# Optimization experiments

Hardware: AMD Instinct MI355X
Metric: run time of the kernel (lower is better)

## Reference

```python
import jax, jax.numpy as jnp
import numpy as np

B, S, H, D = 4, 4096, 1024, 64

def setup_inputs() -> dict:
    key = jax.random.key(0)
    ks = jax.random.split(key, 10)
    return {
        "query": jax.random.normal(ks[0], (B, S, H), jnp.float32),
        "key": jax.random.normal(ks[1], (B, S, H), jnp.float32),
        "value": jax.random.normal(ks[2], (B, S, H), jnp.float32),
        "mask": jax.random.randint(ks[3], (B, S), 0, 2, jnp.int32),
        "Wq": jax.random.normal(ks[4], (H, D), jnp.float32) * 0.02,
        "bq": jax.random.normal(ks[5], (D,), jnp.float32) * 0.02,
        "Wk": jax.random.normal(ks[6], (H, D), jnp.float32) * 0.02,
        "bk": jax.random.normal(ks[7], (D,), jnp.float32) * 0.02,
        "Wv": jax.random.normal(ks[8], (H, D), jnp.float32) * 0.02,
        "bv": jax.random.normal(ks[9], (D,), jnp.float32) * 0.02,
    }

def reference(query, key, value, mask, Wq, bq, Wk, bk, Wv, bv):
    # single-head projections: [B,S,H] @ [H,D] -> [B,S,D]
    q = query @ Wq + bq
    k = key @ Wk + bk
    v = value @ Wv + bv
    scale = 1.0 / np.sqrt(D).astype(np.float32)
    # [B,Sq,Sk] score matrix (faithful to the unfused original)
    scores = jnp.einsum('bqd,bkd->bqk', q, k) * scale
    # mask [B,Sk] broadcast over query dim; masked positions -> -1e9
    scores = jnp.where(mask[:, None, :] == 0, jnp.float32(-1e9), scores)
    att = jax.nn.softmax(scores, axis=-1)
    # dropout prob = 0.0 -> identity
    return jnp.einsum('bqk,bkd->bqd', att, v)
```

## Files before the change

kernel.cpp:

```cpp
#include <hip/hip_runtime.h>
#include <hip/hip_bf16.h>
#include <stdint.h>


typedef __bf16 bf16;
typedef __bf16 bf16x8 __attribute__((ext_vector_type(8)));
typedef float f32x16 __attribute__((ext_vector_type(16)));

union B8 { uint4 u; bf16x8 v; uint32_t w[4]; };

#define AS1 __attribute__((address_space(1)))
#define AS3 __attribute__((address_space(3)))

__device__ __forceinline__ void async16(const void* g, void* l) {
  __builtin_amdgcn_global_load_lds((AS1 void*)(g), (AS3 void*)(l), 16, 0, 0);
}

#define KSC 0.18033688011112042f

__global__ void setup_kernel(const float* __restrict__ Wq, const float* __restrict__ Wk,
                             const float* __restrict__ Wv, const int* __restrict__ mask,
                             bf16* __restrict__ wT, float* __restrict__ biasArr)
{
  int item = blockIdx.x * 256 + threadIdx.x;
  if (item < 24576) {
    int mat = item >> 13;
    int rem = item & 8191;
    int n   = rem >> 7;
    int c   = rem & 127;
    const float* W = (mat == 0) ? Wq : (mat == 1) ? Wk : Wv;
    union { bf16 b[8]; uint4 u; } pk;
    #pragma unroll
    for (int j = 0; j < 8; ++j)
      pk.b[j] = (bf16)W[(c * 8 + j) * 64 + n];
    bf16* o = wT + mat * 65536;
    *(uint4*)(o + n * 1024 + c * 8) = pk.u;
  } else {
    int i = (item - 24576) << 2;
    const int4 m = *(const int4*)(mask + i);
    float4 b;
    b.x = m.x ? 0.0f : -1e30f;
    b.y = m.y ? 0.0f : -1e30f;
    b.z = m.z ? 0.0f : -1e30f;
    b.w = m.w ? 0.0f : -1e30f;
    *(float4*)(biasArr + i) = b;
  }
}

__global__ __launch_bounds__(128) void proj_kernel(
    const float* __restrict__ Xq, const float* __restrict__ Xk, const float* __restrict__ Xv,
    const bf16* __restrict__ wT,
    const float* __restrict__ bq, const float* __restrict__ bk, const float* __restrict__ bv,
    bf16* __restrict__ qo, bf16* __restrict__ ko, bf16* __restrict__ vTo)
{
  const int bx = blockIdx.x;
  const int mat = bx >> 9;
  const int m0 = (bx & 511) << 5;
  const float* X    = (mat == 0) ? Xq : (mat == 1) ? Xk : Xv;
  const float* bias = (mat == 0) ? bq : (mat == 1) ? bk : bv;
  const bf16* w = wT + mat * 65536;

  __shared__ __align__(16) float xbuf[2][32 * 64];
  __shared__ __align__(16) bf16 cs[32 * 64];

  const int tid  = threadIdx.x;
  const int wv   = tid >> 6;
  const int lane = tid & 63;
  const int half = lane >> 5;
  const int ln   = lane & 31;

  const int drow = lane >> 4;
  const int dcl  = lane & 15;

  const float* xb = X + (size_t)m0 * 1024;
  const bf16*  w0 = w + ((wv << 5) + ln) * 1024 + half * 8;

  float b0v = bias[(wv << 5) + ln];

  float4 sx0, sx1, sx2, sx3;
  uint4  sw0, sw1, sw2, sw3;
  uint4  cw0, cw1, cw2, cw3;

  #define LX1(dst, i_, j)                                                  \
    { int ii_ = (wv << 2) + (i_);                                          \
      int row_ = ii_ * 4 + drow;                                           \
      int sc_ = (dcl & 8) | ((dcl ^ (row_ & 7)) & 7);                      \
      dst = *(const float4*)(xb + (size_t)(j) * 64 + (size_t)row_ * 1024 + sc_ * 4); }
  #define LOADX(j)  LX1(sx0, 0, j) LX1(sx1, 1, j) LX1(sx2, 2, j) LX1(sx3, 3, j)

  #define LW1(dst, s_, j)  { dst = *(const uint4*)(w0 + (j) * 64 + (s_) * 16); }
  #define LOADW_S(j) LW1(sw0, 0, j) LW1(sw1, 1, j) LW1(sw2, 2, j) LW1(sw3, 3, j)
  #define LOADW_C(j) LW1(cw0, 0, j) LW1(cw1, 1, j) LW1(cw2, 2, j) LW1(cw3, 3, j)

  #define WX1(src, i_, dptr)                                               \
    { int ii_ = (wv << 2) + (i_);                                          \
      *(float4*)((dptr) + ii_ * 256 + lane * 4) = src; }
  #define WRITEX(dptr) WX1(sx0, 0, dptr) WX1(sx1, 1, dptr) WX1(sx2, 2, dptr) WX1(sx3, 3, dptr)

  #define CST(s_, WREG)                                                    \
    { int lc_ = (s_) * 4 + half * 2;                                       \
      int p0_ = (lc_ & 8) | ((lc_ ^ (ln & 7)) & 7);                        \
      int p1_ = ((lc_ + 1) & 8) | (((lc_ + 1) ^ (ln & 7)) & 7);            \
      float4 fa_ = *(const float4*)(xl + ln * 64 + p0_ * 4);               \
      float4 fb_ = *(const float4*)(xl + ln * 64 + p1_ * 4);               \
      union { bf16 b[8]; bf16x8 v; } af_;                                  \
      af_.b[0] = (bf16)fa_.x; af_.b[1] = (bf16)fa_.y;                      \
      af_.b[2] = (bf16)fa_.z; af_.b[3] = (bf16)fa_.w;                      \
      af_.b[4] = (bf16)fb_.x; af_.b[5] = (bf16)fb_.y;                      \
      af_.b[6] = (bf16)fb_.z; af_.b[7] = (bf16)fb_.w;                      \
      B8 wa_; wa_.u = WREG;                                                \
      acc = __builtin_amdgcn_mfma_f32_32x32x16_bf16(af_.v, wa_.v, acc, 0, 0, 0); }

  LOADX(0);
  LOADW_C(0);
  { float* dp = &xbuf[0][0]; WRITEX(dp); }
  asm volatile("s_waitcnt lgkmcnt(0)" ::: "memory");
  __builtin_amdgcn_s_barrier();

  f32x16 acc = {};

  for (int c = 0; c < 16; ++c) {
    if (c < 15) {
      LOADX(c + 1);
      LOADW_S(c + 1);
    }
    const float* xl = &xbuf[c & 1][0];
    CST(0, cw0) CST(1, cw1) CST(2, cw2) CST(3, cw3)
    if (c < 15) {
      { float* dp = &xbuf[(c + 1) & 1][0]; WRITEX(dp); }
      asm volatile("s_waitcnt lgkmcnt(0)" ::: "memory");
      __builtin_amdgcn_s_barrier();
      cw0 = sw0; cw1 = sw1; cw2 = sw2; cw3 = sw3;
    }
  }

  #undef LX1
  #undef LOADX
  #undef LW1
  #undef LOADW_S
  #undef LOADW_C
  #undef WX1
  #undef WRITEX
  #undef CST

  #pragma unroll
  for (int r = 0; r < 16; ++r) {
    int mrow = (r & 3) + 8 * (r >> 2) + 4 * half;
    cs[mrow * 64 + (wv << 5) + ln] = (bf16)(acc[r] + b0v);
  }
  __syncthreads();

  if (mat < 2) {
    bf16* gout = (mat == 0) ? qo : ko;
    #pragma unroll
    for (int p = 0; p < 2; ++p) {
      int id = p * 128 + tid;
      int r = id >> 3;
      int c = id & 7;
      int phys = c ^ (r & 7);
      *(uint4*)(gout + (size_t)(m0 + r) * 64 + phys * 8) = *(const uint4*)(cs + r * 64 + c * 8);
    }
  } else {
    int batch = m0 >> 12;
    int sk = m0 & 4095;
    int tb = sk & ~63;
    int halfTile = (sk >> 5) & 1;
    #pragma unroll
    for (int p = 0; p < 2; ++p) {
      int id = p * 128 + tid;
      int d = id >> 2;
      int j = id & 3;
      union { bf16 b[8]; uint4 u; } pk;
      #pragma unroll
      for (int t = 0; t < 8; ++t) pk.b[t] = cs[(j * 8 + t) * 64 + d];
      int cl = halfTile * 4 + j;
      int phys = cl ^ (d & 7);
      *(uint4*)(vTo + ((size_t)batch * 64 + d) * 4096 + tb + phys * 8) = pk.u;
    }
  }
}

__global__ __launch_bounds__(256, 2) void flash_kernel(
    const bf16* __restrict__ qb, const bf16* __restrict__ kb, const bf16* __restrict__ vT,
    const float* __restrict__ biasArr, float* __restrict__ out)
{
  __shared__ __align__(16) char smem[65536];
  bf16* ksb = (bf16*)smem;
  bf16* vsb = (bf16*)(smem + 32768);

  const int tid = threadIdx.x;
  const int lane = tid & 63;
  const int wv = tid >> 6;
  const int half = lane >> 5;
  const int ln = lane & 31;

  const int batch = blockIdx.x >> 6;
  const int q0 = (blockIdx.x & 63) << 6;

  bf16x8 qf[2][4];
  const bf16* qbase = qb + ((size_t)batch * 4096 + q0) * 64;
  #pragma unroll
  for (int qk = 0; qk < 2; ++qk)
  #pragma unroll
  for (int s = 0; s < 4; ++s) {
    int qq = (qk << 5) + ln;
    int phys = (2 * s + half) ^ (qq & 7);
    B8 t; t.u = *(const uint4*)(qbase + qq * 64 + phys * 8);
    qf[qk][s] = t.v;
  }

  f32x16 acc[2][2] = {{{}, {}}, {{}, {}}};
  float den0 = 0.f, den1 = 0.f;

  bf16* kds = ksb + wv * 4096;
  bf16* vds = vsb + wv * 4096;
  const bf16* kgb = kb + (size_t)batch * 4096 * 64;
  const bf16* vgb = vT + (size_t)batch * 64 * 4096;
  const float* barr = biasArr + batch * 4096;

  for (int it = 0; it < 16; ++it) {
    const int key0 = wv * 1024 + it * 64;
    __syncthreads();
    const bf16* ksrc = kgb + (size_t)key0 * 64;
    #pragma unroll
    for (int i = 0; i < 8; ++i)
      async16((const char*)ksrc + i * 1024 + lane * 16, (char*)kds + i * 1024);
    const bf16* vsrc = vgb + key0;
    #pragma unroll
    for (int i = 0; i < 8; ++i)
      async16((const char*)vsrc + ((size_t)(i * 8 + (lane >> 3)) * 4096 + (lane & 7) * 8) * 2,
              (char*)vds + i * 1024);
    __syncthreads();

    #pragma unroll
    for (int st = 0; st < 2; ++st) {
      f32x16 s0 = {};
      f32x16 s1 = {};
      #pragma unroll
      for (int s = 0; s < 4; ++s) {
        int key = (st << 5) + ln;
        B8 af; af.u = *(const uint4*)(kds + key * 64 + (((2 * s + half) ^ (key & 7)) << 3));
        s0 = __builtin_amdgcn_mfma_f32_32x32x16_bf16(af.v, qf[0][s], s0, 0, 0, 0);
        s1 = __builtin_amdgcn_mfma_f32_32x32x16_bf16(af.v, qf[1][s], s1, 0, 0, 0);
      }
      float bb[16];
      #pragma unroll
      for (int g = 0; g < 4; ++g)
        *(float4*)&bb[4 * g] = *(const float4*)(barr + key0 + (st << 5) + 8 * g + (half << 2));
      uint32_t pk0[8], pk1[8];
      #pragma unroll
      for (int i = 0; i < 8; ++i) {
        float a0 = __builtin_amdgcn_exp2f(fmaf(s0[2 * i],     KSC, bb[2 * i]));
        float a1 = __builtin_amdgcn_exp2f(fmaf(s0[2 * i + 1], KSC, bb[2 * i + 1]));
        float c0 = __builtin_amdgcn_exp2f(fmaf(s1[2 * i],     KSC, bb[2 * i]));
        float c1 = __builtin_amdgcn_exp2f(fmaf(s1[2 * i + 1], KSC, bb[2 * i + 1]));
        den0 += a0 + a1;
        den1 += c0 + c1;
        union { bf16 b[2]; uint32_t u; } u0, u1;
        u0.b[0] = (bf16)a0; u0.b[1] = (bf16)a1;
        u1.b[0] = (bf16)c0; u1.b[1] = (bf16)c1;
        pk0[i] = u0.u; pk1[i] = u1.u;
      }
      uint32_t xp0[8], xp1[8];
      #pragma unroll
      for (int i = 0; i < 8; ++i) {
        xp0[i] = (uint32_t)__shfl_xor((int)pk0[i], 32);
        xp1[i] = (uint32_t)__shfl_xor((int)pk1[i], 32);
      }
      #pragma unroll
      for (int t = 0; t < 2; ++t) {
        B8 p0f, p1f;
        p0f.w[0] = half ? xp0[4 * t + 2] : pk0[4 * t];
        p0f.w[1] = half ? xp0[4 * t + 3] : pk0[4 * t + 1];
        p0f.w[2] = half ? pk0[4 * t + 2] : xp0[4 * t];
        p0f.w[3] = half ? pk0[4 * t + 3] : xp0[4 * t + 1];
        p1f.w[0] = half ? xp1[4 * t + 2] : pk1[4 * t];
        p1f.w[1] = half ? xp1[4 * t + 3] : pk1[4 * t + 1];
        p1f.w[2] = half ? pk1[4 * t + 2] : xp1[4 * t];
        p1f.w[3] = half ? pk1[4 * t + 3] : xp1[4 * t + 1];
        #pragma unroll
        for (int dh = 0; dh < 2; ++dh) {
          int d = (dh << 5) + ln;
          B8 vf; vf.u = *(const uint4*)(vds + d * 64 +
                          ((((st << 2) + (t << 1) + half) ^ (d & 7)) << 3));
          acc[0][dh] = __builtin_amdgcn_mfma_f32_32x32x16_bf16(vf.v, p0f.v, acc[0][dh], 0, 0, 0);
          acc[1][dh] = __builtin_amdgcn_mfma_f32_32x32x16_bf16(vf.v, p1f.v, acc[1][dh], 0, 0, 0);
        }
      }
    }
  }

  den0 += __shfl_xor(den0, 32);
  den1 += __shfl_xor(den1, 32);

  float* nb = (float*)smem;
  float* dn = (float*)(smem + 34816);

  __syncthreads();
  if (wv >= 2) {
    float* mynb = nb + (wv - 2) * 4352;
    #pragma unroll
    for (int qk = 0; qk < 2; ++qk)
    #pragma unroll
    for (int dh = 0; dh < 2; ++dh)
    #pragma unroll
    for (int g = 0; g < 4; ++g) {
      int q = (qk << 5) + ln;
      int d = 8 * g + (half << 2) + (dh << 5);
      f32x16 a = acc[qk][dh];
      *(float4*)(mynb + q * 68 + d) = make_float4(a[4*g], a[4*g+1], a[4*g+2], a[4*g+3]);
    }
    if (half == 0) {
      dn[(wv - 2) * 64 + ln]      = den0;
      dn[(wv - 2) * 64 + 32 + ln] = den1;
    }
  }
  __syncthreads();
  if (wv < 2) {
    float* pb = nb + wv * 4352;
    #pragma unroll
    for (int qk = 0; qk < 2; ++qk)
    #pragma unroll
    for (int dh = 0; dh < 2; ++dh)
    #pragma unroll
    for (int g = 0; g < 4; ++g) {
      int q = (qk << 5) + ln;
      int d = 8 * g + (half << 2) + (dh << 5);
      float4 t = *(const float4*)(pb + q * 68 + d);
      acc[qk][dh][4*g+0] += t.x; acc[qk][dh][4*g+1] += t.y;
      acc[qk][dh][4*g+2] += t.z; acc[qk][dh][4*g+3] += t.w;
    }
    den0 += dn[wv * 64 + ln];
    den1 += dn[wv * 64 + 32 + ln];
  }
  __syncthreads();
  if (wv < 2) {
    float* mynb = nb + wv * 4352;
    #pragma unroll
    for (int qk = 0; qk < 2; ++qk)
    #pragma unroll
    for (int dh = 0; dh < 2; ++dh)
    #pragma unroll
    for (int g = 0; g < 4; ++g) {
      int q = (qk << 5) + ln;
      int d = 8 * g + (half << 2) + (dh << 5);
      f32x16 a = acc[qk][dh];
      *(float4*)(mynb + q * 68 + d) = make_float4(a[4*g], a[4*g+1], a[4*g+2], a[4*g+3]);
    }
    if (half == 0) {
      dn[wv * 64 + ln]      = den0;
      dn[wv * 64 + 32 + ln] = den1;
    }
  }
  __syncthreads();
  #pragma unroll
  for (int p = 0; p < 4; ++p) {
    int i = p * 256 + tid;
    int qq = i >> 4;
    int d4 = (i & 15) << 2;
    float4 A = *(const float4*)(nb + qq * 68 + d4);
    float4 Bv = *(const float4*)(nb + 4352 + qq * 68 + d4);
    float dd = dn[qq] + dn[64 + qq];
    float inv = 1.0f / dd;
    float4 o = make_float4((A.x + Bv.x) * inv, (A.y + Bv.y) * inv,
                           (A.z + Bv.z) * inv, (A.w + Bv.w) * inv);
    *(float4*)(out + ((size_t)batch * 4096 + q0 + qq) * 64 + d4) = o;
  }
}

extern "C" void kernel_launch(void* const* d_in, const int* in_sizes, int n_in,
                              void* d_out, int out_size, void* d_ws, size_t ws_size,
                              hipStream_t stream)
{
  const float* query = (const float*)d_in[0];
  const float* key   = (const float*)d_in[1];
  const float* value = (const float*)d_in[2];
  const int*   mask  = (const int*)d_in[3];
  const float* Wq    = (const float*)d_in[4];
  const float* bq    = (const float*)d_in[5];
  const float* Wk    = (const float*)d_in[6];
  const float* bk    = (const float*)d_in[7];
  const float* Wv    = (const float*)d_in[8];
  const float* bv    = (const float*)d_in[9];
  float* out = (float*)d_out;

  bf16* qb = (bf16*)d_ws;
  bf16* kb = qb + 1048576;
  bf16* vT = kb + 1048576;
  bf16* wT = vT + 1048576;
  float* biasArr = (float*)((char*)d_ws + 3 * 2097152 + 393216);

  setup_kernel<<<112, 256, 0, stream>>>(Wq, Wk, Wv, mask, wT, biasArr);
  proj_kernel<<<1536, 128, 0, stream>>>(query, key, value, wT, bq, bk, bv, qb, kb, vT);
  flash_kernel<<<256, 256, 0, stream>>>(qb, kb, vT, biasArr, out);
}
```

Measured before the change: 271.5 us.

## Stage full 32x1024 X tile in LDS as bf16 before projection MFMA loop

The projection kernel no longer streams X in 64-column fp32 chunks through a double buffer with a barrier per chunk. Each wave now loads its 16 rows of X with long contiguous per-lane reads, converts them to bf16 once, and writes them into a 64KB swizzled LDS buffer. After a single barrier, the MFMA loop reads ready-made bf16 fragments. This removes 15 barriers and repeated per-chunk conversion, at the cost of 64KB of LDS per block, which limits occupancy, and no overlap between the X load and compute.

```diff
diff --git a/kernel.cpp b/kernel.cpp
--- a/kernel.cpp
+++ b/kernel.cpp
@@ -60,8 +60,8 @@
   const float* bias = (mat == 0) ? bq : (mat == 1) ? bk : bv;
   const bf16* w = wT + mat * 65536;
 
-  __shared__ __align__(16) float xbuf[2][32 * 64];
-  __shared__ __align__(16) bf16 cs[32 * 64];
+  __shared__ __align__(16) char psm[65536];
+  bf16* cs = (bf16*)psm;
 
   const int tid  = threadIdx.x;
   const int wv   = tid >> 6;
@@ -69,79 +69,76 @@
   const int half = lane >> 5;
   const int ln   = lane & 31;
 
-  const int drow = lane >> 4;
-  const int dcl  = lane & 15;
-
-  const float* xb = X + (size_t)m0 * 1024;
-  const bf16*  w0 = w + ((wv << 5) + ln) * 1024 + half * 8;
-
+  const bf16* w0 = w + ((wv << 5) + ln) * 1024 + half * 8;
   float b0v = bias[(wv << 5) + ln];
 
-  float4 sx0, sx1, sx2, sx3;
-  uint4  sw0, sw1, sw2, sw3;
-  uint4  cw0, cw1, cw2, cw3;
-
-  #define LX1(dst, i_, j)                                                  \
-    { int ii_ = (wv << 2) + (i_);                                          \
-      int row_ = ii_ * 4 + drow;                                           \
-      int sc_ = (dcl & 8) | ((dcl ^ (row_ & 7)) & 7);                      \
-      dst = *(const float4*)(xb + (size_t)(j) * 64 + (size_t)row_ * 1024 + sc_ * 4); }
-  #define LOADX(j)  LX1(sx0, 0, j) LX1(sx1, 1, j) LX1(sx2, 2, j) LX1(sx3, 3, j)
-
+  const float* xrow = X + (size_t)(m0 + (wv << 4)) * 1024 + lane * 16;
+  const int c16a = lane * 2;
+  const int c16b = lane * 2 + 1;
+  const int gx   = (lane >> 2) & 7;
+
+  float4 a0, a1, a2, a3, b0, b1, b2, b3;
+
+  #define LDROW(s0, s1, s2, s3, rr)                                        \
+    { const float* p_ = xrow + (size_t)(rr) * 1024;                        \
+      s0 = *(const float4*)(p_);      s1 = *(const float4*)(p_ + 4);       \
+      s2 = *(const float4*)(p_ + 8);  s3 = *(const float4*)(p_ + 12); }
+
+  #define WRROW(s0, s1, s2, s3, rr)                                        \
+    { int r_ = (wv << 4) + (rr);                                           \
+      int pa_ = (c16a & ~7) | ((c16a ^ (r_ & 7) ^ gx) & 7);                \
+      int pb_ = (c16b & ~7) | ((c16b ^ (r_ & 7) ^ gx) & 7);                \
+      union { bf16 b[8]; uint4 q; } ua_, ub_;                              \
+      ua_.b[0] = (bf16)s0.x; ua_.b[1] = (bf16)s0.y;                        \
+      ua_.b[2] = (bf16)s0.z; ua_.b[3] = (bf16)s0.w;                        \
+      ua_.b[4] = (bf16)s1.x; ua_.b[5] = (bf16)s1.y;                        \
+      ua_.b[6] = (bf16)s1.z; ua_.b[7] = (bf16)s1.w;                        \
+      ub_.b[0] = (bf16)s2.x; ub_.b[1] = (bf16)s2.y;                        \
+      ub_.b[2] = (bf16)s2.z; ub_.b[3] = (bf16)s2.w;                        \
+      ub_.b[4] = (bf16)s3.x; ub_.b[5] = (bf16)s3.y;                        \
+      ub_.b[6] = (bf16)s3.z; ub_.b[7] = (bf16)s3.w;                        \
+      *(uint4*)(psm + r_ * 2048 + pa_ * 16) = ua_.q;                       \
+      *(uint4*)(psm + r_ * 2048 + pb_ * 16) = ub_.q; }
+
+  LDROW(a0, a1, a2, a3, 0)
+  for (int rr = 0; rr < 16; rr += 2) {
+    LDROW(b0, b1, b2, b3, rr + 1)
+    WRROW(a0, a1, a2, a3, rr)
+    if (rr < 14) LDROW(a0, a1, a2, a3, rr + 2)
+    WRROW(b0, b1, b2, b3, rr + 1)
+  }
+  #undef LDROW
+  #undef WRROW
+
+  __syncthreads();
+
+  uint4 cw0, cw1, cw2, cw3, sw0, sw1, sw2, sw3;
   #define LW1(dst, s_, j)  { dst = *(const uint4*)(w0 + (j) * 64 + (s_) * 16); }
+  #define LOADW_C(j) LW1(cw0, 0, j) LW1(cw1, 1, j) LW1(cw2, 2, j) LW1(cw3, 3, j)
   #define LOADW_S(j) LW1(sw0, 0, j) LW1(sw1, 1, j) LW1(sw2, 2, j) LW1(sw3, 3, j)
-  #define LOADW_C(j) LW1(cw0, 0, j) LW1(cw1, 1, j) LW1(cw2, 2, j) LW1(cw3, 3, j)
-
-  #define WX1(src, i_, dptr)                                               \
-    { int ii_ = (wv << 2) + (i_);                                          \
-      *(float4*)((dptr) + ii_ * 256 + lane * 4) = src; }
-  #define WRITEX(dptr) WX1(sx0, 0, dptr) WX1(sx1, 1, dptr) WX1(sx2, 2, dptr) WX1(sx3, 3, dptr)
-
-  #define CST(s_, WREG)                                                    \
-    { int lc_ = (s_) * 4 + half * 2;                                       \
-      int p0_ = (lc_ & 8) | ((lc_ ^ (ln & 7)) & 7);                        \
-      int p1_ = ((lc_ + 1) & 8) | (((lc_ + 1) ^ (ln & 7)) & 7);            \
-      float4 fa_ = *(const float4*)(xl + ln * 64 + p0_ * 4);               \
-      float4 fb_ = *(const float4*)(xl + ln * 64 + p1_ * 4);               \
-      union { bf16 b[8]; bf16x8 v; } af_;                                  \
-      af_.b[0] = (bf16)fa_.x; af_.b[1] = (bf16)fa_.y;                      \
-      af_.b[2] = (bf16)fa_.z; af_.b[3] = (bf16)fa_.w;                      \
-      af_.b[4] = (bf16)fb_.x; af_.b[5] = (bf16)fb_.y;                      \
-      af_.b[6] = (bf16)fb_.z; af_.b[7] = (bf16)fb_.w;                      \
+
+  #define CSTN(c_, s_, WREG)                                               \
+    { int c16_ = (c_) * 8 + (s_) * 2 + half;                               \
+      int phys_ = (c16_ & ~7) | ((c16_ ^ (ln & 7) ^ ((c_) & 7)) & 7);      \
+      B8 af_; af_.u = *(const uint4*)(psm + ln * 2048 + phys_ * 16);       \
       B8 wa_; wa_.u = WREG;                                                \
       acc = __builtin_amdgcn_mfma_f32_32x32x16_bf16(af_.v, wa_.v, acc, 0, 0, 0); }
 
-  LOADX(0);
+  f32x16 acc = {};
+
   LOADW_C(0);
-  { float* dp = &xbuf[0][0]; WRITEX(dp); }
-  asm volatile("s_waitcnt lgkmcnt(0)" ::: "memory");
-  __builtin_amdgcn_s_barrier();
-
-  f32x16 acc = {};
-
   for (int c = 0; c < 16; ++c) {
-    if (c < 15) {
-      LOADX(c + 1);
-      LOADW_S(c + 1);
-    }
-    const float* xl = &xbuf[c & 1][0];
-    CST(0, cw0) CST(1, cw1) CST(2, cw2) CST(3, cw3)
-    if (c < 15) {
-      { float* dp = &xbuf[(c + 1) & 1][0]; WRITEX(dp); }
-      asm volatile("s_waitcnt lgkmcnt(0)" ::: "memory");
-      __builtin_amdgcn_s_barrier();
-      cw0 = sw0; cw1 = sw1; cw2 = sw2; cw3 = sw3;
-    }
-  }
-
-  #undef LX1
-  #undef LOADX
+    if (c < 15) { LOADW_S(c + 1) }
+    CSTN(c, 0, cw0) CSTN(c, 1, cw1) CSTN(c, 2, cw2) CSTN(c, 3, cw3)
+    if (c < 15) { cw0 = sw0; cw1 = sw1; cw2 = sw2; cw3 = sw3; }
+  }
+
   #undef LW1
+  #undef LOADW_C
   #undef LOADW_S
-  #undef LOADW_C
-  #undef WX1
-  #undef WRITEX
-  #undef CST
+  #undef CSTN
+
+  __syncthreads();
 
   #pragma unroll
   for (int r = 0; r < 16; ++r) {
```

Result: no change. 276.3 us (+1.8%).

## Enlarge projection tile to 64 rows and stage weights in shared memory

Applied to the files above, without the earlier changes.

The projection kernel now computes 64x64 output tiles with 256 threads, so each block reads half as many weight passes per activation row. Both the X and W chunks are staged through double-buffered swizzled LDS, and X is converted to bf16 before the LDS write rather than after the read. The weight matrix was previously loaded straight from global into registers by each wave. This cuts redundant weight traffic and LDS bytes, but uses more LDS per block and launches fewer blocks.

```diff
diff --git a/kernel.cpp b/kernel.cpp
--- a/kernel.cpp
+++ b/kernel.cpp
@@ -47,106 +47,113 @@
   }
 }
 
-__global__ __launch_bounds__(128) void proj_kernel(
+__global__ __launch_bounds__(256) void proj_kernel(
     const float* __restrict__ Xq, const float* __restrict__ Xk, const float* __restrict__ Xv,
     const bf16* __restrict__ wT,
     const float* __restrict__ bq, const float* __restrict__ bk, const float* __restrict__ bv,
     bf16* __restrict__ qo, bf16* __restrict__ ko, bf16* __restrict__ vTo)
 {
   const int bx = blockIdx.x;
-  const int mat = bx >> 9;
-  const int m0 = (bx & 511) << 5;
+  const int mat = bx >> 8;
+  const int m0 = (bx & 255) << 6;
   const float* X    = (mat == 0) ? Xq : (mat == 1) ? Xk : Xv;
   const float* bias = (mat == 0) ? bq : (mat == 1) ? bk : bv;
-  const bf16* w = wT + mat * 65536;
-
-  __shared__ __align__(16) float xbuf[2][32 * 64];
-  __shared__ __align__(16) bf16 cs[32 * 64];
+  const bf16* wm = wT + mat * 65536;
+
+  __shared__ __align__(16) char xsm[2][8192];
+  __shared__ __align__(16) char wsm[2][8192];
+  __shared__ __align__(16) bf16 cs[64 * 64];
 
   const int tid  = threadIdx.x;
   const int wv   = tid >> 6;
   const int lane = tid & 63;
   const int half = lane >> 5;
   const int ln   = lane & 31;
+  const int wr   = wv >> 1;
+  const int wc   = wv & 1;
 
   const int drow = lane >> 4;
   const int dcl  = lane & 15;
-
-  const float* xb = X + (size_t)m0 * 1024;
-  const bf16*  w0 = w + ((wv << 5) + ln) * 1024 + half * 8;
-
-  float b0v = bias[(wv << 5) + ln];
+  const int r0   = (wv << 4) + drow;
+  const float* xp = X + (size_t)(m0 + r0) * 1024 + dcl * 4;
+
+  const int wn0 = (wv << 4) + (lane >> 3);
+  const int wj  = lane & 7;
+  const bf16* wp0 = wm + (size_t)wn0 * 1024 + wj * 8;
+
+  const int ar  = (wr << 5) + ln;
+  const int an  = (wc << 5) + ln;
+  const int ar7 = ar & 7;
+  const int an7 = an & 7;
+
+  float b0v = bias[an];
 
   float4 sx0, sx1, sx2, sx3;
-  uint4  sw0, sw1, sw2, sw3;
-  uint4  cw0, cw1, cw2, cw3;
-
-  #define LX1(dst, i_, j)                                                  \
-    { int ii_ = (wv << 2) + (i_);                                          \
-      int row_ = ii_ * 4 + drow;                                           \
-      int sc_ = (dcl & 8) | ((dcl ^ (row_ & 7)) & 7);                      \
-      dst = *(const float4*)(xb + (size_t)(j) * 64 + (size_t)row_ * 1024 + sc_ * 4); }
-  #define LOADX(j)  LX1(sx0, 0, j) LX1(sx1, 1, j) LX1(sx2, 2, j) LX1(sx3, 3, j)
-
-  #define LW1(dst, s_, j)  { dst = *(const uint4*)(w0 + (j) * 64 + (s_) * 16); }
-  #define LOADW_S(j) LW1(sw0, 0, j) LW1(sw1, 1, j) LW1(sw2, 2, j) LW1(sw3, 3, j)
-  #define LOADW_C(j) LW1(cw0, 0, j) LW1(cw1, 1, j) LW1(cw2, 2, j) LW1(cw3, 3, j)
-
-  #define WX1(src, i_, dptr)                                               \
-    { int ii_ = (wv << 2) + (i_);                                          \
-      *(float4*)((dptr) + ii_ * 256 + lane * 4) = src; }
-  #define WRITEX(dptr) WX1(sx0, 0, dptr) WX1(sx1, 1, dptr) WX1(sx2, 2, dptr) WX1(sx3, 3, dptr)
-
-  #define CST(s_, WREG)                                                    \
-    { int lc_ = (s_) * 4 + half * 2;                                       \
-      int p0_ = (lc_ & 8) | ((lc_ ^ (ln & 7)) & 7);                        \
-      int p1_ = ((lc_ + 1) & 8) | (((lc_ + 1) ^ (ln & 7)) & 7);            \
-      float4 fa_ = *(const float4*)(xl + ln * 64 + p0_ * 4);               \
-      float4 fb_ = *(const float4*)(xl + ln * 64 + p1_ * 4);               \
-      union { bf16 b[8]; bf16x8 v; } af_;                                  \
-      af_.b[0] = (bf16)fa_.x; af_.b[1] = (bf16)fa_.y;                      \
-      af_.b[2] = (bf16)fa_.z; af_.b[3] = (bf16)fa_.w;                      \
-      af_.b[4] = (bf16)fb_.x; af_.b[5] = (bf16)fb_.y;                      \
-      af_.b[6] = (bf16)fb_.z; af_.b[7] = (bf16)fb_.w;                      \
-      B8 wa_; wa_.u = WREG;                                                \
-      acc = __builtin_amdgcn_mfma_f32_32x32x16_bf16(af_.v, wa_.v, acc, 0, 0, 0); }
-
-  LOADX(0);
-  LOADW_C(0);
-  { float* dp = &xbuf[0][0]; WRITEX(dp); }
+  uint4  sw0, sw1;
+
+  #define LOADX(j) { const float* p_ = xp + (j) * 64;                       \
+      sx0 = *(const float4*)(p_);                                           \
+      sx1 = *(const float4*)(p_ + 4096);                                    \
+      sx2 = *(const float4*)(p_ + 8192);                                    \
+      sx3 = *(const float4*)(p_ + 12288); }
+
+  #define LOADW(j) { const bf16* q_ = wp0 + (j) * 64;                       \
+      sw0 = *(const uint4*)(q_);                                            \
+      sw1 = *(const uint4*)(q_ + 8192); }
+
+  #define WX1(s_, i_) { int rl_ = r0 + (i_) * 4;                            \
+      int byte_ = rl_ * 128 + (((dcl >> 1) ^ (rl_ & 7)) << 4) + ((dcl & 1) << 3); \
+      union { bf16 b[4]; uint2 u; } pk_;                                    \
+      pk_.b[0] = (bf16)(s_).x; pk_.b[1] = (bf16)(s_).y;                     \
+      pk_.b[2] = (bf16)(s_).z; pk_.b[3] = (bf16)(s_).w;                     \
+      *(uint2*)(dst_ + byte_) = pk_.u; }
+
+  #define WRITEX(bufp) { char* dst_ = (bufp);                               \
+      WX1(sx0, 0) WX1(sx1, 1) WX1(sx2, 2) WX1(sx3, 3) }
+
+  #define WRITEW(bufp) { char* dw_ = (bufp);                                \
+      *(uint4*)(dw_ + wn0 * 128 + ((wj ^ (wn0 & 7)) << 4)) = sw0;           \
+      int n1_ = wn0 + 8;                                                    \
+      *(uint4*)(dw_ + n1_ * 128 + ((wj ^ (n1_ & 7)) << 4)) = sw1; }
+
+  #define COMPUTE(xbp, wbp) { const char* xq_ = (xbp); const char* wq_ = (wbp); \
+      _Pragma("unroll")                                                     \
+      for (int s_ = 0; s_ < 4; ++s_) {                                      \
+        int c16_ = 2 * s_ + half;                                           \
+        B8 af_; af_.u = *(const uint4*)(xq_ + ar * 128 + ((c16_ ^ ar7) << 4)); \
+        B8 wf_; wf_.u = *(const uint4*)(wq_ + an * 128 + ((c16_ ^ an7) << 4)); \
+        acc = __builtin_amdgcn_mfma_f32_32x32x16_bf16(af_.v, wf_.v, acc, 0, 0, 0); } }
+
+  f32x16 acc = {};
+
+  LOADX(0) LOADW(0)
+  WRITEX(xsm[0]) WRITEW(wsm[0])
   asm volatile("s_waitcnt lgkmcnt(0)" ::: "memory");
   __builtin_amdgcn_s_barrier();
-
-  f32x16 acc = {};
+  asm volatile("" ::: "memory");
 
   for (int c = 0; c < 16; ++c) {
+    if (c < 15) { LOADX(c + 1) LOADW(c + 1) }
+    COMPUTE(xsm[c & 1], wsm[c & 1])
     if (c < 15) {
-      LOADX(c + 1);
-      LOADW_S(c + 1);
-    }
-    const float* xl = &xbuf[c & 1][0];
-    CST(0, cw0) CST(1, cw1) CST(2, cw2) CST(3, cw3)
-    if (c < 15) {
-      { float* dp = &xbuf[(c + 1) & 1][0]; WRITEX(dp); }
+      WRITEX(xsm[(c + 1) & 1]) WRITEW(wsm[(c + 1) & 1])
       asm volatile("s_waitcnt lgkmcnt(0)" ::: "memory");
       __builtin_amdgcn_s_barrier();
-      cw0 = sw0; cw1 = sw1; cw2 = sw2; cw3 = sw3;
-    }
-  }
-
-  #undef LX1
+      asm volatile("" ::: "memory");
+    }
+  }
+
   #undef LOADX
-  #undef LW1
-  #undef LOADW_S
-  #undef LOADW_C
+  #undef LOADW
   #undef WX1
   #undef WRITEX
-  #undef CST
+  #undef WRITEW
+  #undef COMPUTE
 
   #pragma unroll
   for (int r = 0; r < 16; ++r) {
     int mrow = (r & 3) + 8 * (r >> 2) + 4 * half;
-    cs[mrow * 64 + (wv << 5) + ln] = (bf16)(acc[r] + b0v);
+    cs[((wr << 5) + mrow) * 64 + an] = (bf16)(acc[r] + b0v);
   }
   __syncthreads();
 
@@ -154,28 +161,24 @@
     bf16* gout = (mat == 0) ? qo : ko;
     #pragma unroll
     for (int p = 0; p < 2; ++p) {
-      int id = p * 128 + tid;
+      int id = p * 256 + tid;
       int r = id >> 3;
       int c = id & 7;
-      int phys = c ^ (r & 7);
-      *(uint4*)(gout + (size_t)(m0 + r) * 64 + phys * 8) = *(const uint4*)(cs + r * 64 + c * 8);
+      *(uint4*)(gout + (size_t)(m0 + r) * 64 + (c ^ (r & 7)) * 8) =
+          *(const uint4*)(cs + r * 64 + c * 8);
     }
   } else {
     int batch = m0 >> 12;
-    int sk = m0 & 4095;
-    int tb = sk & ~63;
-    int halfTile = (sk >> 5) & 1;
+    int tb = m0 & 4095;
     #pragma unroll
     for (int p = 0; p < 2; ++p) {
-      int id = p * 128 + tid;
-      int d = id >> 2;
-      int j = id & 3;
+      int id = p * 256 + tid;
+      int d = id >> 3;
+      int j = id & 7;
       union { bf16 b[8]; uint4 u; } pk;
       #pragma unroll
       for (int t = 0; t < 8; ++t) pk.b[t] = cs[(j * 8 + t) * 64 + d];
-      int cl = halfTile * 4 + j;
-      int phys = cl ^ (d & 7);
-      *(uint4*)(vTo + ((size_t)batch * 64 + d) * 4096 + tb + phys * 8) = pk.u;
+      *(uint4*)(vTo + ((size_t)batch * 64 + d) * 4096 + tb + (j ^ (d & 7)) * 8) = pk.u;
     }
   }
 }
@@ -391,6 +394,6 @@
   float* biasArr = (float*)((char*)d_ws + 3 * 2097152 + 393216);
 
   setup_kernel<<<112, 256, 0, stream>>>(Wq, Wk, Wv, mask, wT, biasArr);
-  proj_kernel<<<1536, 128, 0, stream>>>(query, key, value, wT, bq, bk, bv, qb, kb, vT);
+  proj_kernel<<<768, 256, 0, stream>>>(query, key, value, wT, bq, bk, bv, qb, kb, vT);
   flash_kernel<<<256, 256, 0, stream>>>(qb, kb, vT, biasArr, out);
 }
```

After: 259.6 us. 1.05x faster.
